# Optimization experiments

Measured on AMD Instinct MI355X. Metric: run time of the kernel, lower is better.

The kernel has to match this reference:

```python
import jax, jax.numpy as jnp
import numpy as np

B, N, E, L, G, F, H = 64, 500, 16000, 64, 64, 8, 128

def setup_inputs() -> dict:
    key = jax.random.key(0)
    ks = jax.random.split(key, 8)
    return {
        "x": jax.random.normal(ks[0], (B, N, L), dtype=jnp.float32),
        "incidence": jax.random.normal(ks[1], (N, E), dtype=jnp.float32),
        "ef": jax.random.normal(ks[2], (E, F), dtype=jnp.float32),
        "W1": jax.random.normal(ks[3], (F, H), dtype=jnp.float32) * 0.1,
        "b1": jax.random.normal(ks[4], (H,), dtype=jnp.float32) * 0.1,
        "W2": jax.random.normal(ks[5], (H, L * G), dtype=jnp.float32) * 0.1,
        "b2": jax.random.normal(ks[6], (L * G,), dtype=jnp.float32) * 0.1,
        "b_gc": jax.random.normal(ks[7], (G,), dtype=jnp.float32) * 0.1,
    }

def reference(x, incidence, ef, W1, b1, W2, b2, b_gc):
    # MLP-generated per-edge kernel: [E, G, L]
    h = jax.nn.relu(ef @ W1 + b1)
    kernel = (h @ W2 + b2).reshape(E, G, L)
    # gather node features onto edges: [B, E, L]
    t = jnp.einsum('bnl,ne->bel', x, incidence)
    # per-edge batched matvec: [B, E, G]
    y = jnp.einsum('egl,bel->beg', kernel, t)
    # scatter back to nodes: [B, N, G]
    y = jnp.einsum('ne,beg->bng', incidence, y)
    # gc is a frozen identity Linear -> just add bias, then ReLU
    y = jax.nn.relu(y + b_gc)
    return y.reshape(x.shape[0], -1)
```

## Files before the change

### kernel.cpp

```cpp
#include <hip/hip_runtime.h>

constexpr int B_ = 64, N_ = 500, E_ = 16000, L_ = 64, G_ = 64, F_ = 8, H_ = 128;
constexpr int GL_ = 4096;
constexpr int NP_ = 512;
constexpr int KS_ = 4;
constexpr int ACC_ELEMS = B_ * N_ * G_;

using bf16x8  = __attribute__((ext_vector_type(8))) short;
using f32x4   = __attribute__((ext_vector_type(4))) float;
using ushort8 = __attribute__((ext_vector_type(8))) unsigned short;

#define MFMA16(a, b, c) __builtin_amdgcn_mfma_f32_16x16x32_bf16((a), (b), (c), 0, 0, 0)

typedef __attribute__((address_space(3))) unsigned int       lds_u32;
typedef const __attribute__((address_space(1))) unsigned int glb_u32;

static __device__ __forceinline__ unsigned short f2bf(float f) {
    union { float f; unsigned u; } v; v.f = f;
    unsigned r = v.u + 0x7fffu + ((v.u >> 16) & 1u);
    return (unsigned short)(r >> 16);
}
static __device__ __forceinline__ float bf2f(unsigned short s) {
    union { float f; unsigned u; } v; v.u = ((unsigned)s) << 16;
    return v.f;
}

static __device__ __forceinline__ void stage_tile(
    const unsigned short* __restrict__ g, int ld, int r0, int kk,
    unsigned short* lds, int tid)
{
    #pragma unroll
    for (int c = 0; c < 4; ++c) {
        const int ch  = tid + c * 256;
        const int row = ch >> 3;
        const int csw = (ch & 7) ^ (row & 7);
        __builtin_amdgcn_global_load_lds(
            (glb_u32*)(g + (size_t)(r0 + row) * ld + kk + csw * 8),
            (lds_u32*)(lds + (size_t)ch * 8), 16, 0, 0);
    }
}

static __device__ __forceinline__ void gemm_body(
    const unsigned short* __restrict__ A, int lda,
    const unsigned short* __restrict__ Bm, int ldb,
    int K, int nN,
    unsigned short* __restrict__ C, int ldc,
    const float* __restrict__ bias)
{
    const int nwg = gridDim.x;
    const int bid = blockIdx.x;
    const int swz = (nwg & 7) ? bid : ((bid & 7) * (nwg >> 3) + (bid >> 3));
    const int m0 = (swz / nN) * 128, n0 = (swz % nN) * 128;

    const int tid  = threadIdx.x;
    const int lane = tid & 63, wid = tid >> 6;
    const int wm = wid >> 1, wn = wid & 1;
    const int fr = lane & 15, fq = lane >> 4;

    __shared__ __align__(16) unsigned short smem[4 * 128 * 64];
    unsigned short* const As0 = smem;
    unsigned short* const Bs0 = smem + 128 * 64;
    unsigned short* const As1 = smem + 2 * 128 * 64;
    unsigned short* const Bs1 = smem + 3 * 128 * 64;

    const f32x4 fz = {0.f, 0.f, 0.f, 0.f};
    f32x4 acc[4][4] = {{fz, fz, fz, fz}, {fz, fz, fz, fz},
                       {fz, fz, fz, fz}, {fz, fz, fz, fz}};

    const int rowA[4] = {wm * 64 + 0 * 16 + fr, wm * 64 + 1 * 16 + fr,
                         wm * 64 + 2 * 16 + fr, wm * 64 + 3 * 16 + fr};
    const int rowB[4] = {wn * 64 + 0 * 16 + fr, wn * 64 + 1 * 16 + fr,
                         wn * 64 + 2 * 16 + fr, wn * 64 + 3 * 16 + fr};

    const int nk = K / 64;
    stage_tile(A, lda, m0, 0, As0, tid);
    stage_tile(Bm, ldb, n0, 0, Bs0, tid);

    for (int kt = 0; kt < nk; ++kt) {
        unsigned short* const Ac = (kt & 1) ? As1 : As0;
        unsigned short* const Bc = (kt & 1) ? Bs1 : Bs0;
        if (kt + 1 < nk) {
            unsigned short* const An = (kt & 1) ? As0 : As1;
            unsigned short* const Bn = (kt & 1) ? Bs0 : Bs1;
            stage_tile(A, lda, m0, (kt + 1) * 64, An, tid);
            stage_tile(Bm, ldb, n0, (kt + 1) * 64, Bn, tid);
            asm volatile("s_waitcnt vmcnt(8)" ::: "memory");
        } else {
            asm volatile("s_waitcnt vmcnt(0)" ::: "memory");
        }
        __builtin_amdgcn_s_barrier();
        __builtin_amdgcn_sched_barrier(0);
        #pragma unroll
        for (int ks = 0; ks < 2; ++ks) {
            bf16x8 af[4], bf[4];
            #pragma unroll
            for (int i = 0; i < 4; ++i)
                af[i] = *(const bf16x8*)&Ac[rowA[i] * 64 +
                         (((ks * 4 + fq) ^ (rowA[i] & 7)) * 8)];
            #pragma unroll
            for (int j = 0; j < 4; ++j)
                bf[j] = *(const bf16x8*)&Bc[rowB[j] * 64 +
                         (((ks * 4 + fq) ^ (rowB[j] & 7)) * 8)];
            #pragma unroll
            for (int i = 0; i < 4; ++i)
                #pragma unroll
                for (int j = 0; j < 4; ++j)
                    acc[i][j] = MFMA16(af[i], bf[j], acc[i][j]);
        }
        __builtin_amdgcn_sched_barrier(0);
        __builtin_amdgcn_s_barrier();
    }

    auto Cs = (unsigned short(*)[128])smem;
    #pragma unroll
    for (int i = 0; i < 4; ++i)
        #pragma unroll
        for (int j = 0; j < 4; ++j) {
            const float bv = bias ? bias[n0 + wn * 64 + j * 16 + fr] : 0.f;
            #pragma unroll
            for (int r = 0; r < 4; ++r)
                Cs[wm * 64 + i * 16 + fq * 4 + r][wn * 64 + j * 16 + fr] =
                    f2bf(acc[i][j][r] + bv);
        }
    __syncthreads();
    const int r2 = tid >> 4, o2 = (tid & 15) * 8;
    #pragma unroll
    for (int i = 0; i < 8; ++i) {
        const int row = i * 16 + r2;
        *(uint4*)&C[(size_t)(m0 + row) * ldc + n0 + o2] = *(const uint4*)&Cs[row][o2];
    }
}

__global__ __launch_bounds__(256)
void gemm_pair(const unsigned short* __restrict__ A0, int lda0,
               const unsigned short* __restrict__ B0, int ldb0, int K0,
               unsigned short* __restrict__ C0, const float* __restrict__ bias0,
               const unsigned short* __restrict__ A1, int lda1,
               const unsigned short* __restrict__ B1, int ldb1, int K1,
               unsigned short* __restrict__ C1, int nN)
{
    if (blockIdx.y == 0)
        gemm_body(A0, lda0, B0, ldb0, K0, nN, C0, GL_, bias0);
    else
        gemm_body(A1, lda1, B1, ldb1, K1, nN, C1, GL_, nullptr);
}

__global__ __launch_bounds__(512)
void k_y8(unsigned short* tc, const unsigned short* __restrict__ Kc)
{
    const int e0 = blockIdx.x * 8;
    const int tid = threadIdx.x, lane = tid & 63, w = tid >> 6;
    const int e = e0 + w;
    const int fr = lane & 15, fq = lane >> 4;
    const unsigned short* A  = &tc[(size_t)e * GL_];
    const unsigned short* Bp = &Kc[(size_t)e * GL_];
    const f32x4 fz = {0.f, 0.f, 0.f, 0.f};
    f32x4 acc[4][4] = {{fz, fz, fz, fz}, {fz, fz, fz, fz},
                       {fz, fz, fz, fz}, {fz, fz, fz, fz}};
    #pragma unroll
    for (int ks = 0; ks < 2; ++ks) {
        bf16x8 af[4], bf[4];
        #pragma unroll
        for (int i = 0; i < 4; ++i)
            af[i] = *(const bf16x8*)&A[(i * 16 + fr) * 64 + ks * 32 + fq * 8];
        #pragma unroll
        for (int j = 0; j < 4; ++j)
            bf[j] = *(const bf16x8*)&Bp[(j * 16 + fr) * 64 + ks * 32 + fq * 8];
        #pragma unroll
        for (int i = 0; i < 4; ++i)
            #pragma unroll
            for (int j = 0; j < 4; ++j)
                acc[i][j] = MFMA16(af[i], bf[j], acc[i][j]);
    }
    __shared__ unsigned short y8[GL_ * 8];
    #pragma unroll
    for (int i = 0; i < 4; ++i)
        #pragma unroll
        for (int j = 0; j < 4; ++j)
            #pragma unroll
            for (int r = 0; r < 4; ++r) {
                const int bg = (i * 16 + fq * 4 + r) * 64 + j * 16 + fr;
                y8[bg * 8 + w] = f2bf(acc[i][j][r]);
            }
    __syncthreads();
    unsigned short* dst = tc + (size_t)e0 * GL_;
    #pragma unroll
    for (int p = 0; p < 8; ++p) {
        const int o = (p * 512 + tid) * 8;
        *(uint4*)&dst[o] = *(const uint4*)&y8[o];
    }
}

__global__ __launch_bounds__(256)
void k_accd(const unsigned short* __restrict__ Ae,
            const unsigned short* __restrict__ y8,
            unsigned short* __restrict__ planesB, int pbase, int K)
{
    const int xcd = blockIdx.x & 7, grp = blockIdx.x >> 3;
    const int m0 = (grp & 7) * 64;
    const int n0 = (xcd + 8 * (grp >> 3)) * 128;
    const int KSY = gridDim.y;
    const int kl = ((K / KSY) / 64) * 64;
    const int kbeg = blockIdx.y * kl;
    const int kend = ((int)blockIdx.y == KSY - 1) ? K : kbeg + kl;

    const int lane = threadIdx.x & 63, wid = threadIdx.x >> 6;
    const int wm = wid >> 1, wn = wid & 1;
    const int fr = lane & 15, fq = lane >> 4;

    const f32x4 fz = {0.f, 0.f, 0.f, 0.f};
    f32x4 acc[2][4] = {{fz, fz, fz, fz}, {fz, fz, fz, fz}};

    for (int kk = kbeg; kk < kend; kk += 64) {
        #pragma unroll
        for (int ks = 0; ks < 2; ++ks) {
            const int e8 = kk + ks * 32 + fq * 8;
            const size_t eb = (size_t)(e8 >> 3);
            bf16x8 af[2], bf[4];
            #pragma unroll
            for (int i = 0; i < 2; ++i)
                af[i] = *(const bf16x8*)&Ae[(eb * NP_ + m0 + wm * 32 + i * 16 + fr) * 8];
            #pragma unroll
            for (int j = 0; j < 4; ++j)
                bf[j] = *(const bf16x8*)&y8[eb * GL_ * 8 + (n0 + wn * 64 + j * 16 + fr) * 8];
            #pragma unroll
            for (int i = 0; i < 2; ++i)
                #pragma unroll
                for (int j = 0; j < 4; ++j)
                    acc[i][j] = MFMA16(af[i], bf[j], acc[i][j]);
        }
    }

    unsigned short* pl = planesB + (size_t)(pbase + blockIdx.y) * ACC_ELEMS;
    #pragma unroll
    for (int i = 0; i < 2; ++i)
        #pragma unroll
        for (int j = 0; j < 4; ++j) {
            const int col = n0 + wn * 64 + j * 16 + fr;
            const int b = col >> 6, g = col & 63;
            #pragma unroll
            for (int r = 0; r < 4; ++r) {
                const int n = m0 + wm * 32 + i * 16 + fq * 4 + r;
                if (n < N_)
                    pl[((size_t)b * N_ + n) * G_ + g] = f2bf(acc[i][j][r]);
            }
        }
}

__global__ __launch_bounds__(256)
void k_cvt_inc(const float* __restrict__ inc, unsigned short* __restrict__ incT,
               unsigned short* __restrict__ incB8)
{
    const int e0 = blockIdx.x * 64, n0 = blockIdx.y * 64;
    const int tid = threadIdx.x, cl = tid & 63;
    __shared__ unsigned short sm[64][80];
    for (int rr = tid >> 6; rr < 64; rr += 4) {
        const int n = n0 + rr;
        sm[cl][rr] = (n < N_) ? f2bf(inc[(size_t)n * E_ + e0 + cl]) : (unsigned short)0;
    }
    __syncthreads();
    {
        const int cw = tid >> 2, j0 = (tid & 3) * 16;
        *(ushort8*)&incT[(size_t)(e0 + cw) * NP_ + n0 + j0]     = *(const ushort8*)&sm[cw][j0];
        *(ushort8*)&incT[(size_t)(e0 + cw) * NP_ + n0 + j0 + 8] = *(const ushort8*)&sm[cw][j0 + 8];
    }
    {
        const int eb = tid >> 5, idx = tid & 31;
        #pragma unroll
        for (int k = 0; k < 2; ++k) {
            const int row = idx * 2 + k;
            unsigned short tmp[8];
            #pragma unroll
            for (int q = 0; q < 8; ++q) tmp[q] = sm[eb * 8 + q][row];
            *(ushort8*)&incB8[((size_t)((e0 >> 3) + eb) * NP_ + n0 + row) * 8] =
                *(const ushort8*)&tmp[0];
        }
    }
}

__global__ __launch_bounds__(256)
void k_tr32(const float* __restrict__ in, unsigned short* __restrict__ out,
            int R, int C, int Rp, size_t inZ, size_t outZ)
{
    in  += (size_t)blockIdx.z * inZ;
    out += (size_t)blockIdx.z * outZ;
    const int c0 = blockIdx.x * 64, r0 = blockIdx.y * 64;
    __shared__ float sm[64][65];
    const int cl = threadIdx.x & 63;
    for (int rr = threadIdx.x >> 6; rr < 64; rr += 4) {
        const int r = r0 + rr;
        sm[cl][rr] = (r < R) ? in[(size_t)r * C + c0 + cl] : 0.f;
    }
    __syncthreads();
    const int cw = threadIdx.x >> 2, j0 = (threadIdx.x & 3) * 16;
    unsigned short tmp[16];
    #pragma unroll
    for (int j = 0; j < 16; ++j) tmp[j] = f2bf(sm[cw][j0 + j]);
    *(ushort8*)&out[(size_t)(c0 + cw) * Rp + r0 + j0]     = *(ushort8*)&tmp[0];
    *(ushort8*)&out[(size_t)(c0 + cw) * Rp + r0 + j0 + 8] = *(ushort8*)&tmp[8];
}

__global__ __launch_bounds__(256)
void k_h(const float* __restrict__ ef, const float* __restrict__ W1,
         const float* __restrict__ b1, unsigned short* __restrict__ h)
{
    const int idx = blockIdx.x * 256 + threadIdx.x;
    const int e = idx >> 7, hh = idx & 127;
    float v = b1[hh];
    const float* efp = &ef[(size_t)e * F_];
    #pragma unroll
    for (int f = 0; f < F_; ++f) v += efp[f] * W1[f * H_ + hh];
    h[idx] = f2bf(fmaxf(v, 0.f));
}

__global__ __launch_bounds__(256)
void k_final(const unsigned short* __restrict__ planesB, int P,
             const float* __restrict__ bgc, float* __restrict__ out)
{
    const int i = (blockIdx.x * 256 + threadIdx.x) * 8;
    if (i >= ACC_ELEMS) return;
    float s[8];
    #pragma unroll
    for (int j = 0; j < 8; ++j) s[j] = bgc[(i + j) & 63];
    for (int p = 0; p < P; ++p) {
        const ushort8 v = *(const ushort8*)&planesB[(size_t)p * ACC_ELEMS + i];
        #pragma unroll
        for (int j = 0; j < 8; ++j) s[j] += bf2f((unsigned short)v[j]);
    }
    float4 o0, o1;
    o0.x = fmaxf(s[0], 0.f); o0.y = fmaxf(s[1], 0.f);
    o0.z = fmaxf(s[2], 0.f); o0.w = fmaxf(s[3], 0.f);
    o1.x = fmaxf(s[4], 0.f); o1.y = fmaxf(s[5], 0.f);
    o1.z = fmaxf(s[6], 0.f); o1.w = fmaxf(s[7], 0.f);
    *(float4*)&out[i]     = o0;
    *(float4*)&out[i + 4] = o1;
}

extern "C" void kernel_launch(void* const* d_in, const int* in_sizes, int n_in,
                              void* d_out, int out_size, void* d_ws, size_t ws_size,
                              hipStream_t stream) {
    const float* x   = (const float*)d_in[0];
    const float* inc = (const float*)d_in[1];
    const float* ef  = (const float*)d_in[2];
    const float* W1  = (const float*)d_in[3];
    const float* b1  = (const float*)d_in[4];
    const float* W2  = (const float*)d_in[5];
    const float* b2  = (const float*)d_in[6];
    const float* bgc = (const float*)d_in[7];
    float* out = (float*)d_out;

    const size_t persistU16 = (size_t)NP_ * E_
                            + (size_t)E_ * NP_
                            + (size_t)B_ * L_ * NP_
                            + (size_t)E_ * H_
                            + (size_t)GL_ * H_;
    const size_t persistBytes = persistU16 * 2;

    int nc = 1, Ec = E_;
    for (; nc <= 16; ++nc) {
        Ec = ((E_ + nc - 1) / nc + 127) / 128 * 128;
        const size_t need = persistBytes
                          + (size_t)nc * KS_ * ACC_ELEMS * 2
                          + 2 * (size_t)Ec * GL_ * 2;
        if (need <= ws_size) break;
    }
    if (nc > 16) { nc = 16; Ec = 1024; }

    unsigned short* planesB = (unsigned short*)d_ws;
    unsigned short* incB8 = planesB + (size_t)nc * KS_ * ACC_ELEMS;
    unsigned short* incT = incB8 + (size_t)NP_ * E_;
    unsigned short* xT   = incT + (size_t)E_ * NP_;
    unsigned short* h    = xT   + (size_t)B_ * L_ * NP_;
    unsigned short* W2T  = h    + (size_t)E_ * H_;
    unsigned short* Kc   = W2T  + (size_t)GL_ * H_;
    unsigned short* tc   = Kc   + (size_t)Ec * GL_;

    k_cvt_inc<<<dim3(E_ / 64, NP_ / 64), 256, 0, stream>>>(inc, incT, incB8);
    k_tr32<<<dim3(1, NP_ / 64, B_),      256, 0, stream>>>(x, xT, N_, L_, NP_,
                                                           (size_t)N_ * L_, (size_t)L_ * NP_);
    k_tr32<<<dim3(GL_ / 64, H_ / 64, 1), 256, 0, stream>>>(W2, W2T, H_, GL_, H_, 0, 0);
    k_h<<<dim3(E_ * H_ / 256), 256, 0, stream>>>(ef, W1, b1, h);

    int cidx = 0;
    for (int e_off = 0; e_off < E_; e_off += Ec, ++cidx) {
        const int ec = (E_ - e_off) < Ec ? (E_ - e_off) : Ec;
        gemm_pair<<<dim3((ec / 128) * 32, 2), 256, 0, stream>>>(
            h + (size_t)e_off * H_, H_, W2T, H_, H_, Kc, b2,
            incT + (size_t)e_off * NP_, NP_, xT, NP_, NP_, tc, 32);
        k_y8<<<dim3(ec / 8), 512, 0, stream>>>(tc, Kc);
        k_accd<<<dim3(256, KS_), 256, 0, stream>>>(
            incB8 + (size_t)e_off * NP_, tc, planesB, cidx * KS_, ec);
    }

    k_final<<<dim3(ACC_ELEMS / 2048), 256, 0, stream>>>(planesB, nc * KS_, bgc, out);
}
```

Before: 373.2 us.

## Switch GEMM mainloop to triple-buffered K=32 stages with prefetch depth two

The GEMM body previously double-buffered 64-wide K tiles. It now uses three LDS buffers of 32-wide K tiles, with a new swizzle pattern and precomputed column offsets, and prefetches two stages ahead. The goal is to hide global-to-LDS load latency better while cutting LDS use from 64KB to 48KB, which may allow more resident workgroups. In exchange there are twice as many barrier iterations, with less MFMA work per barrier.

```diff
diff --git a/kernel.cpp b/kernel.cpp
--- a/kernel.cpp
+++ b/kernel.cpp
@@ -25,15 +25,15 @@
     return v.f;
 }
 
-static __device__ __forceinline__ void stage_tile(
+static __device__ __forceinline__ void stage32(
     const unsigned short* __restrict__ g, int ld, int r0, int kk,
     unsigned short* lds, int tid)
 {
     #pragma unroll
-    for (int c = 0; c < 4; ++c) {
+    for (int c = 0; c < 2; ++c) {
         const int ch  = tid + c * 256;
-        const int row = ch >> 3;
-        const int csw = (ch & 7) ^ (row & 7);
+        const int row = ch >> 2;
+        const int csw = (ch & 3) ^ ((row >> 1) & 3);
         __builtin_amdgcn_global_load_lds(
             (glb_u32*)(g + (size_t)(r0 + row) * ld + kk + csw * 8),
             (lds_u32*)(lds + (size_t)ch * 8), 16, 0, 0);
@@ -57,11 +57,7 @@
     const int wm = wid >> 1, wn = wid & 1;
     const int fr = lane & 15, fq = lane >> 4;
 
-    __shared__ __align__(16) unsigned short smem[4 * 128 * 64];
-    unsigned short* const As0 = smem;
-    unsigned short* const Bs0 = smem + 128 * 64;
-    unsigned short* const As1 = smem + 2 * 128 * 64;
-    unsigned short* const Bs1 = smem + 3 * 128 * 64;
+    __shared__ __align__(16) unsigned short smem[3 * 8192];
 
     const f32x4 fz = {0.f, 0.f, 0.f, 0.f};
     f32x4 acc[4][4] = {{fz, fz, fz, fz}, {fz, fz, fz, fz},
@@ -71,36 +67,44 @@
                          wm * 64 + 2 * 16 + fr, wm * 64 + 3 * 16 + fr};
     const int rowB[4] = {wn * 64 + 0 * 16 + fr, wn * 64 + 1 * 16 + fr,
                          wn * 64 + 2 * 16 + fr, wn * 64 + 3 * 16 + fr};
-
-    const int nk = K / 64;
-    stage_tile(A, lda, m0, 0, As0, tid);
-    stage_tile(Bm, ldb, n0, 0, Bs0, tid);
-
+    int cA[4], cB[4];
+    #pragma unroll
+    for (int i = 0; i < 4; ++i) {
+        cA[i] = (fq ^ ((rowA[i] >> 1) & 3)) * 8;
+        cB[i] = (fq ^ ((rowB[i] >> 1) & 3)) * 8;
+    }
+
+    const int nk = K / 32;
+    stage32(A, lda, m0, 0, smem, tid);
+    stage32(Bm, ldb, n0, 0, smem + 4096, tid);
+    stage32(A, lda, m0, 32, smem + 8192, tid);
+    stage32(Bm, ldb, n0, 32, smem + 8192 + 4096, tid);
+
+    int cur = 0;
     for (int kt = 0; kt < nk; ++kt) {
-        unsigned short* const Ac = (kt & 1) ? As1 : As0;
-        unsigned short* const Bc = (kt & 1) ? Bs1 : Bs0;
-        if (kt + 1 < nk) {
-            unsigned short* const An = (kt & 1) ? As0 : As1;
-            unsigned short* const Bn = (kt & 1) ? Bs0 : Bs1;
-            stage_tile(A, lda, m0, (kt + 1) * 64, An, tid);
-            stage_tile(Bm, ldb, n0, (kt + 1) * 64, Bn, tid);
+        unsigned short* const As = smem + cur * 8192;
+        unsigned short* const Bs = As + 4096;
+        if (kt + 2 < nk) {
+            int nxt = cur + 2; if (nxt >= 3) nxt -= 3;
+            unsigned short* const An = smem + nxt * 8192;
+            stage32(A, lda, m0, (kt + 2) * 32, An, tid);
+            stage32(Bm, ldb, n0, (kt + 2) * 32, An + 4096, tid);
             asm volatile("s_waitcnt vmcnt(8)" ::: "memory");
+        } else if (kt + 1 < nk) {
+            asm volatile("s_waitcnt vmcnt(4)" ::: "memory");
         } else {
             asm volatile("s_waitcnt vmcnt(0)" ::: "memory");
         }
         __builtin_amdgcn_s_barrier();
         __builtin_amdgcn_sched_barrier(0);
-        #pragma unroll
-        for (int ks = 0; ks < 2; ++ks) {
+        {
             bf16x8 af[4], bf[4];
             #pragma unroll
             for (int i = 0; i < 4; ++i)
-                af[i] = *(const bf16x8*)&Ac[rowA[i] * 64 +
-                         (((ks * 4 + fq) ^ (rowA[i] & 7)) * 8)];
+                af[i] = *(const bf16x8*)&As[rowA[i] * 32 + cA[i]];
             #pragma unroll
             for (int j = 0; j < 4; ++j)
-                bf[j] = *(const bf16x8*)&Bc[rowB[j] * 64 +
-                         (((ks * 4 + fq) ^ (rowB[j] & 7)) * 8)];
+                bf[j] = *(const bf16x8*)&Bs[rowB[j] * 32 + cB[j]];
             #pragma unroll
             for (int i = 0; i < 4; ++i)
                 #pragma unroll
@@ -109,6 +113,7 @@
         }
         __builtin_amdgcn_sched_barrier(0);
         __builtin_amdgcn_s_barrier();
+        cur = (cur + 1 == 3) ? 0 : cur + 1;
     }
 
     auto Cs = (unsigned short(*)[128])smem;
```

After: 366.6 us. Within noise of the previous version (-1.8%).
